# Kernel optimization log

Measured on AMD Instinct MI355X. Metric: run time of the kernel, lower is better.

The kernel has to match this reference:

```python
import jax, jax.numpy as jnp
import numpy as np

N, D, T, H, R = 1024, 6, 60, 64, 64
NEG = -10000.0
SLOPE = 0.01  # default LeakyReLU negative slope


def setup_inputs() -> dict:
    key = jax.random.key(0)
    ks = jax.random.split(key, 12)
    x = jax.random.normal(ks[0], (N, D * T), jnp.float32)
    relation_matrix = (jax.random.uniform(ks[1], (N, N, R)) < 0.02).astype(jnp.float32)
    s = 1.0 / np.sqrt(H)
    inp = {
        "x": x,
        "relation_matrix": relation_matrix,
        "W": jax.random.normal(ks[2], (2 * H + R, 1), jnp.float32) / np.sqrt(2 * H + R),
        "b": jnp.zeros((), jnp.float32),
        "fc_w": jax.random.normal(ks[3], (1, 2 * H), jnp.float32) * s,
        "fc_b": jnp.zeros((1,), jnp.float32),
        "Wih0": jax.random.normal(ks[4], (3 * H, D), jnp.float32) * s,
        "Whh0": jax.random.normal(ks[5], (3 * H, H), jnp.float32) * s,
        "bih0": jax.random.normal(ks[6], (3 * H,), jnp.float32) * s,
        "bhh0": jax.random.normal(ks[7], (3 * H,), jnp.float32) * s,
        "Wih1": jax.random.normal(ks[8], (3 * H, H), jnp.float32) * s,
        "Whh1": jax.random.normal(ks[9], (3 * H, H), jnp.float32) * s,
        "bih1": jax.random.normal(ks[10], (3 * H,), jnp.float32) * s,
        "bhh1": jax.random.normal(ks[11], (3 * H,), jnp.float32) * s,
    }
    return inp


def gru_layer(x, Wih, Whh, bih, bhh):
    # x: [N, T, in] -> outputs [N, T, H]; torch GRU gate order: r, z, n
    xg = x @ Wih.T + bih            # [N, T, 3H], input gates precomputed
    xg = jnp.swapaxes(xg, 0, 1)     # [T, N, 3H]

    def step(h, g):
        hg = h @ Whh.T + bhh
        xr, xz, xn = jnp.split(g, 3, axis=-1)
        hr, hz, hn = jnp.split(hg, 3, axis=-1)
        r = jax.nn.sigmoid(xr + hr)
        z = jax.nn.sigmoid(xz + hz)
        n = jnp.tanh(xn + r * hn)
        h = (1.0 - z) * n + z * h
        return h, h

    h0 = jnp.zeros((x.shape[0], Whh.shape[1]), x.dtype)
    _, ys = jax.lax.scan(step, h0, xg)
    return jnp.swapaxes(ys, 0, 1)   # [N, T, H]


def reference(x, relation_matrix, W, b, fc_w, fc_b,
              Wih0, Whh0, bih0, bhh0, Wih1, Whh1, bih1, bhh1):
    # [N, D*T] -> [N, T, D]
    xs = jnp.transpose(x.reshape(x.shape[0], D, -1), (0, 2, 1))
    h = gru_layer(xs, Wih0, Whh0, bih0, bhh0)
    h = gru_layer(h, Wih1, Whh1, bih1, bhh1)
    h = h[:, -1, :]                 # [N, H] last-step hidden

    # score[i,j] = cat(h_i, h_j, rel_ij) @ W + b, computed without the NxNx(2H+R) concat
    Wv = W[:, 0]
    sa = h @ Wv[:H]                              # [N]  (ei part)
    sb = h @ Wv[H:2 * H]                         # [N]  (hidden_batch part)
    sr = jnp.einsum('ijr,r->ij', relation_matrix, Wv[2 * H:])  # [N, N]
    weight = sa[:, None] + sb[None, :] + sr + b
    weight = jnp.where(weight >= 0, weight, SLOPE * weight)    # LeakyReLU

    mask = (relation_matrix.sum(-1) != 0).astype(h.dtype)      # [N, N]
    temp = mask * weight
    temp = jnp.where(temp == 0, NEG, temp)                     # faithful to torch ==0 fill
    valid = jax.nn.softmax(temp, axis=1) * mask

    agg = valid @ h                                            # [N, H]
    hidden = jnp.concatenate([h, agg], axis=1)                 # [N, 2H]
    pred_all = (hidden @ fc_w.T + fc_b).squeeze()
    return pred_all
```

## Files before the change

### kernel.cpp

```cpp
#include <hip/hip_runtime.h>
#include <cstddef>

#define NN 1024
#define DD 6
#define TT 60
#define HH 64
#define NEGV  (-10000.0f)
#define SLOPEV (0.01f)
#define GRUB 64
#define RELB 896

#define PRZ 0
#define PXN 2432
#define PHN 3648
#define HF0 4864
#define HF1 6080
#define BH0 7296
#define BH1 7872
#define XH  8448
#define SMEMF 12288

typedef _Float16 v8h __attribute__((ext_vector_type(8)));
typedef float    v4f __attribute__((ext_vector_type(4)));

#define MF(a, b, c) __builtin_amdgcn_mfma_f32_16x16x32_f16((a), (b), (c), 0, 0, 0)

__device__ __forceinline__ float sig_(float x)  { return 1.0f / (1.0f + __expf(-x)); }
__device__ __forceinline__ float tanh_(float x) { return 1.0f - 2.0f / (__expf(2.0f * x) + 1.0f); }
__device__ __forceinline__ float bcf_(const float a, const float b) {
    return __builtin_bit_cast(float, __builtin_amdgcn_cvt_pkrtz(a, b));
}
__device__ __forceinline__ v8h zero8() {
    v8h r;
    #pragma unroll
    for (int j = 0; j < 8; ++j) r[j] = (_Float16)0.f;
    return r;
}
__device__ __forceinline__ v8h pack8(const float* __restrict__ p) {
    v8h r;
    #pragma unroll
    for (int j = 0; j < 8; ++j) r[j] = (_Float16)p[j];
    return r;
}
__device__ __forceinline__ v8h pack6(const float* __restrict__ p) {
    v8h r = zero8();
    #pragma unroll
    for (int j = 0; j < 6; ++j) r[j] = (_Float16)p[j];
    return r;
}

__global__ __launch_bounds__(256, 1)
void k_main(const float* __restrict__ x, const float* __restrict__ rel,
            const float* __restrict__ W, const float* __restrict__ fc_w,
            const float* __restrict__ Wih0, const float* __restrict__ Whh0,
            const float* __restrict__ bih0, const float* __restrict__ bhh0,
            const float* __restrict__ Wih1, const float* __restrict__ Whh1,
            const float* __restrict__ bih1, const float* __restrict__ bhh1,
            float* __restrict__ sa, float* __restrict__ sb,
            float* __restrict__ hdot, float* __restrict__ hb,
            float* __restrict__ sr, float* __restrict__ ssum)
{
    __shared__ float smem[SMEMF];
    const int tid = threadIdx.x;

    if (blockIdx.x >= GRUB) {
        const float* __restrict__ Wv = W + 2 * HH;
        const unsigned base = (unsigned)(blockIdx.x - GRUB) * 256 + tid;
        for (unsigned p = base; p < (unsigned)(NN * NN); p += (unsigned)RELB * 256) {
            const float4* b4 = (const float4*)(rel + (size_t)p * 64);
            float4 v[16];
            #pragma unroll
            for (int q = 0; q < 16; ++q) v[q] = b4[q];
            float d0 = 0.f, d1 = 0.f, s0 = 0.f, s1 = 0.f;
            #pragma unroll
            for (int q = 0; q < 16; ++q) {
                d0 += v[q].x * Wv[4*q]   + v[q].z * Wv[4*q+2];
                d1 += v[q].y * Wv[4*q+1] + v[q].w * Wv[4*q+3];
                s0 += v[q].x + v[q].z;
                s1 += v[q].y + v[q].w;
            }
            sr[p]   = d0 + d1;
            ssum[p] = s0 + s1;
        }
        return;
    }

    const int w    = tid >> 6;
    const int lane = tid & 63;
    const int quad = lane >> 4;
    const int mc   = lane & 15;
    const int nb   = blockIdx.x * 16;

    for (int idx = tid; idx < TT * 16; idx += 256) {
        const int t = idx >> 4, n = idx & 15;
        const float* xp = x + (size_t)(nb + n) * (DD * TT) + t;
        float4 pk;
        pk.x = bcf_(xp[0],   xp[60]);
        pk.y = bcf_(xp[120], xp[180]);
        pk.z = bcf_(xp[240], xp[300]);
        pk.w = 0.f;
        *(float4*)(smem + XH + idx * 4) = pk;
    }
    for (int idx = tid; idx < 1152; idx += 256) smem[BH0 + idx] = 0.f;
    for (int idx = tid; idx < 2432; idx += 256) smem[HF0 + idx] = 0.f;

    const int r0row = 16 * w + mc;
    const int zrow  = 64 + 16 * w + mc;
    const int nrow  = 128 + 16 * w + mc;
    const v8h Ar0 = pack8(Whh0 + (size_t)r0row * HH + quad * 8);
    const v8h Ar1 = pack8(Whh0 + (size_t)r0row * HH + 32 + quad * 8);
    const v8h Az0 = pack8(Whh0 + (size_t)zrow  * HH + quad * 8);
    const v8h Az1 = pack8(Whh0 + (size_t)zrow  * HH + 32 + quad * 8);
    const v8h An0 = pack8(Whh0 + (size_t)nrow  * HH + quad * 8);
    const v8h An1 = pack8(Whh0 + (size_t)nrow  * HH + 32 + quad * 8);
    v8h Arx = zero8(), Azx = zero8(), Anx = zero8();
    if (quad == 0) {
        Arx = pack6(Wih0 + r0row * DD);
        Azx = pack6(Wih0 + zrow  * DD);
        Anx = pack6(Wih0 + nrow  * DD);
    }
    const v8h R0 = pack8(Wih1 + (size_t)r0row * HH + quad * 8);
    const v8h R1 = pack8(Wih1 + (size_t)r0row * HH + 32 + quad * 8);
    const v8h R2 = pack8(Whh1 + (size_t)r0row * HH + quad * 8);
    const v8h R3 = pack8(Whh1 + (size_t)r0row * HH + 32 + quad * 8);
    const v8h Z0 = pack8(Wih1 + (size_t)zrow * HH + quad * 8);
    const v8h Z1 = pack8(Wih1 + (size_t)zrow * HH + 32 + quad * 8);
    const v8h Z2 = pack8(Whh1 + (size_t)zrow * HH + quad * 8);
    const v8h Z3 = pack8(Whh1 + (size_t)zrow * HH + 32 + quad * 8);
    const v8h Nx0 = pack8(Wih1 + (size_t)nrow * HH + quad * 8);
    const v8h Nx1 = pack8(Wih1 + (size_t)nrow * HH + 32 + quad * 8);
    const v8h Nh0 = pack8(Whh1 + (size_t)nrow * HH + quad * 8);
    const v8h Nh1 = pack8(Whh1 + (size_t)nrow * HH + 32 + quad * 8);

    float bR0[4], bZ0v[4], bXn0[4], bHn0[4], bR1[4], bZ1v[4], bXn1[4], bHn1[4];
    #pragma unroll
    for (int e = 0; e < 4; ++e) {
        const int cr = 16 * w + quad * 4 + e;
        bR0[e]  = bih0[cr] + bhh0[cr];
        bZ0v[e] = bih0[64 + cr] + bhh0[64 + cr];
        bXn0[e] = bih0[128 + cr];
        bHn0[e] = bhh0[128 + cr];
        bR1[e]  = bih1[cr] + bhh1[cr];
        bZ1v[e] = bih1[64 + cr] + bhh1[64 + cr];
        bXn1[e] = bih1[128 + cr];
        bHn1[e] = bhh1[128 + cr];
    }
    __syncthreads();

    auto ldb = [&](int BH, int win) -> v8h {
        return __builtin_bit_cast(v8h,
            *(const float4*)(smem + BH + mc * 36 + win * 16 + quad * 4));
    };
    auto stC = [&](int base, int rowbase, v4f c) {
        #pragma unroll
        for (int e = 0; e < 4; ++e)
            smem[base + (rowbase + quad * 4 + e) * 19 + mc] = c[e];
    };
    auto upd = [&](int HF, int BH) {
        const int n = tid & 15, jb = (tid >> 4) * 4;
        float hv[4];
        #pragma unroll
        for (int e = 0; e < 4; ++e) {
            const int j = jb + e;
            const float rp = smem[PRZ + j * 19 + n];
            const float zp = smem[PRZ + (64 + j) * 19 + n];
            const float xn = smem[PXN + j * 19 + n];
            const float hn = smem[PHN + j * 19 + n];
            const float hp = smem[HF + j * 19 + n];
            const float r  = sig_(rp), z = sig_(zp);
            const float nv = tanh_(xn + r * hn);
            const float h  = (1.f - z) * nv + z * hp;
            smem[HF + j * 19 + n] = h;
            hv[e] = h;
        }
        float2 pk;
        pk.x = bcf_(hv[0], hv[1]);
        pk.y = bcf_(hv[2], hv[3]);
        *(float2*)(smem + BH + n * 36 + (jb >> 1)) = pk;
    };

    for (int t = 0; t < TT; ++t) {
        {
            const v8h b0 = ldb(BH0, 0);
            const v8h b1 = ldb(BH0, 1);
            const float4 xl = *(const float4*)(smem + XH + (t * 16 + mc) * 4);
            v8h bx = zero8();
            if (quad == 0) bx = __builtin_bit_cast(v8h, xl);

            v4f c = {bR0[0], bR0[1], bR0[2], bR0[3]};
            c = MF(Ar0, b0, c); c = MF(Ar1, b1, c); c = MF(Arx, bx, c);
            stC(PRZ, 16 * w, c);
            v4f cz = {bZ0v[0], bZ0v[1], bZ0v[2], bZ0v[3]};
            cz = MF(Az0, b0, cz); cz = MF(Az1, b1, cz); cz = MF(Azx, bx, cz);
            stC(PRZ, 64 + 16 * w, cz);
            v4f ch = {bHn0[0], bHn0[1], bHn0[2], bHn0[3]};
            ch = MF(An0, b0, ch); ch = MF(An1, b1, ch);
            stC(PHN, 16 * w, ch);
            v4f cx = {bXn0[0], bXn0[1], bXn0[2], bXn0[3]};
            cx = MF(Anx, bx, cx);
            stC(PXN, 16 * w, cx);
        }
        __syncthreads();
        upd(HF0, BH0);
        __syncthreads();
        {
            const v8h g0 = ldb(BH0, 0);
            const v8h g1 = ldb(BH0, 1);
            const v8h g2 = ldb(BH1, 0);
            const v8h g3 = ldb(BH1, 1);

            v4f c = {bR1[0], bR1[1], bR1[2], bR1[3]};
            c = MF(R0, g0, c); c = MF(R1, g1, c); c = MF(R2, g2, c); c = MF(R3, g3, c);
            stC(PRZ, 16 * w, c);
            v4f cz = {bZ1v[0], bZ1v[1], bZ1v[2], bZ1v[3]};
            cz = MF(Z0, g0, cz); cz = MF(Z1, g1, cz); cz = MF(Z2, g2, cz); cz = MF(Z3, g3, cz);
            stC(PRZ, 64 + 16 * w, cz);
            v4f cx = {bXn1[0], bXn1[1], bXn1[2], bXn1[3]};
            cx = MF(Nx0, g0, cx); cx = MF(Nx1, g1, cx);
            stC(PXN, 16 * w, cx);
            v4f ch = {bHn1[0], bHn1[1], bHn1[2], bHn1[3]};
            ch = MF(Nh0, g2, ch); ch = MF(Nh1, g3, ch);
            stC(PHN, 16 * w, ch);
        }
        __syncthreads();
        upd(HF1, BH1);
        __syncthreads();
    }

    {
        const int n = lane >> 2, p = lane & 3;
        const float* __restrict__ wp = (w == 0) ? W : (w == 1) ? (W + HH)
                                     : (w == 2) ? fc_w : (fc_w + HH);
        float v = 0.f;
        #pragma unroll
        for (int q = 0; q < 16; ++q) {
            const int j = p * 16 + q;
            v += smem[HF1 + j * 19 + n] * wp[j];
        }
        v += __shfl_down(v, 2);
        v += __shfl_down(v, 1);
        if (p == 0) {
            float* dst = (w == 0) ? sa : (w == 1) ? sb : (w == 2) ? hdot : hb;
            dst[nb + n] = v;
        }
    }
}

__global__ __launch_bounds__(256)
void k2(const float* __restrict__ sa, const float* __restrict__ sb,
        const float* __restrict__ hdot, const float* __restrict__ hb,
        const float* __restrict__ sr, const float* __restrict__ ssum,
        const float* __restrict__ bscal, const float* __restrict__ fc_b,
        float* __restrict__ out)
{
    __shared__ float red[12];
    const int i   = blockIdx.x;
    const int tid = threadIdx.x;
    const int j4  = tid * 4;
    const float sai = sa[i] + bscal[0];

    const float4 srv = *(const float4*)(sr   + (size_t)i * NN + j4);
    const float4 ssv = *(const float4*)(ssum + (size_t)i * NN + j4);
    const float4 sbv = *(const float4*)(sb + j4);

    float tv[4], mk[4];
    float mloc = -3.4e38f;
    {
        const float srq[4] = {srv.x, srv.y, srv.z, srv.w};
        const float ssq[4] = {ssv.x, ssv.y, ssv.z, ssv.w};
        const float sbq[4] = {sbv.x, sbv.y, sbv.z, sbv.w};
        #pragma unroll
        for (int q = 0; q < 4; ++q) {
            float wv = sai + sbq[q] + srq[q];
            wv = (wv >= 0.0f) ? wv : SLOPEV * wv;
            const float m = (ssq[q] != 0.0f) ? 1.0f : 0.0f;
            float tt = m * wv;
            tt = (tt == 0.0f) ? NEGV : tt;
            tv[q] = tt; mk[q] = m;
            mloc = fmaxf(mloc, tt);
        }
    }
    #pragma unroll
    for (int off = 32; off >= 1; off >>= 1) mloc = fmaxf(mloc, __shfl_xor(mloc, off));
    if ((tid & 63) == 0) red[tid >> 6] = mloc;
    __syncthreads();
    const float mx = fmaxf(fmaxf(red[0], red[1]), fmaxf(red[2], red[3]));

    const float4 hbv = *(const float4*)(hb + j4);
    const float hbq[4] = {hbv.x, hbv.y, hbv.z, hbv.w};
    float sloc = 0.0f, vloc = 0.0f;
    #pragma unroll
    for (int q = 0; q < 4; ++q) {
        const float e = __expf(tv[q] - mx);
        sloc += e;
        vloc += e * mk[q] * hbq[q];
    }
    #pragma unroll
    for (int off = 32; off >= 1; off >>= 1) {
        sloc += __shfl_xor(sloc, off);
        vloc += __shfl_xor(vloc, off);
    }
    if ((tid & 63) == 0) { red[4 + (tid >> 6)] = sloc; red[8 + (tid >> 6)] = vloc; }
    __syncthreads();
    if (tid == 0) {
        const float denom = red[4] + red[5] + red[6] + red[7];
        const float vsum  = red[8] + red[9] + red[10] + red[11];
        out[i] = hdot[i] + vsum / denom + fc_b[0];
    }
}

extern "C" void kernel_launch(void* const* d_in, const int* in_sizes, int n_in,
                              void* d_out, int out_size, void* d_ws, size_t ws_size,
                              hipStream_t stream)
{
    const float* x     = (const float*)d_in[0];
    const float* rel   = (const float*)d_in[1];
    const float* W     = (const float*)d_in[2];
    const float* b     = (const float*)d_in[3];
    const float* fc_w  = (const float*)d_in[4];
    const float* fc_b  = (const float*)d_in[5];
    const float* Wih0  = (const float*)d_in[6];
    const float* Whh0  = (const float*)d_in[7];
    const float* bih0  = (const float*)d_in[8];
    const float* bhh0  = (const float*)d_in[9];
    const float* Wih1  = (const float*)d_in[10];
    const float* Whh1  = (const float*)d_in[11];
    const float* bih1  = (const float*)d_in[12];
    const float* bhh1  = (const float*)d_in[13];

    float* ws   = (float*)d_ws;
    float* sa   = ws;
    float* sb   = sa   + NN;
    float* hdot = sb   + NN;
    float* hb   = hdot + NN;
    float* sr   = hb   + NN;
    float* ssum = sr   + (size_t)NN * NN;

    k_main<<<GRUB + RELB, 256, 0, stream>>>(x, rel, W, fc_w,
                                            Wih0, Whh0, bih0, bhh0,
                                            Wih1, Whh1, bih1, bhh1,
                                            sa, sb, hdot, hb, sr, ssum);
    k2<<<NN, 256, 0, stream>>>(sa, sb, hdot, hb, sr, ssum,
                               b, fc_b, (float*)d_out);
}
```

Measured before the change: 436.0 us.

## Pipeline GRU layers across wavefront groups with 512-thread blocks

Doubles the block to 512 threads. Warps 0-3 run GRU layer 0 at step i while warps 4-7 run layer 1 at step i-1, each with its own preactivation buffers in shared memory. This halves the number of barrier phases per timestep, removing the serial dependence between the two layers within a step. The relation-reduction blocks also grow to 512 threads, which raises register pressure with no minimum-occupancy hint and increases shared memory per block.

```diff
diff --git a/kernel.cpp b/kernel.cpp
--- a/kernel.cpp
+++ b/kernel.cpp
@@ -10,15 +10,18 @@
 #define GRUB 64
 #define RELB 896
 
-#define PRZ 0
-#define PXN 2432
-#define PHN 3648
-#define HF0 4864
-#define HF1 6080
-#define BH0 7296
-#define BH1 7872
-#define XH  8448
-#define SMEMF 12288
+#define PA_RZ 0
+#define PA_XN 2432
+#define PA_HN 3648
+#define PB_RZ 4864
+#define PB_XN 7296
+#define PB_HN 8512
+#define HF0   9728
+#define HF1   10944
+#define BH0   12160
+#define BH1   12736
+#define XH    13312
+#define SMEMF 17152
 
 typedef _Float16 v8h __attribute__((ext_vector_type(8)));
 typedef float    v4f __attribute__((ext_vector_type(4)));
@@ -49,7 +52,7 @@
     return r;
 }
 
-__global__ __launch_bounds__(256, 1)
+__global__ __launch_bounds__(512)
 void k_main(const float* __restrict__ x, const float* __restrict__ rel,
             const float* __restrict__ W, const float* __restrict__ fc_w,
             const float* __restrict__ Wih0, const float* __restrict__ Whh0,
@@ -65,8 +68,8 @@
 
     if (blockIdx.x >= GRUB) {
         const float* __restrict__ Wv = W + 2 * HH;
-        const unsigned base = (unsigned)(blockIdx.x - GRUB) * 256 + tid;
-        for (unsigned p = base; p < (unsigned)(NN * NN); p += (unsigned)RELB * 256) {
+        const unsigned base = (unsigned)(blockIdx.x - GRUB) * 512 + tid;
+        for (unsigned p = base; p < (unsigned)(NN * NN); p += (unsigned)RELB * 512) {
             const float4* b4 = (const float4*)(rel + (size_t)p * 64);
             float4 v[16];
             #pragma unroll
@@ -90,8 +93,10 @@
     const int quad = lane >> 4;
     const int mc   = lane & 15;
     const int nb   = blockIdx.x * 16;
-
-    for (int idx = tid; idx < TT * 16; idx += 256) {
+    const bool isL0 = (w < 4);
+    const int wt   = isL0 ? w : (w - 4);
+
+    for (int idx = tid; idx < TT * 16; idx += 512) {
         const int t = idx >> 4, n = idx & 15;
         const float* xp = x + (size_t)(nb + n) * (DD * TT) + t;
         float4 pk;
@@ -101,49 +106,58 @@
         pk.w = 0.f;
         *(float4*)(smem + XH + idx * 4) = pk;
     }
-    for (int idx = tid; idx < 1152; idx += 256) smem[BH0 + idx] = 0.f;
-    for (int idx = tid; idx < 2432; idx += 256) smem[HF0 + idx] = 0.f;
-
-    const int r0row = 16 * w + mc;
-    const int zrow  = 64 + 16 * w + mc;
-    const int nrow  = 128 + 16 * w + mc;
-    const v8h Ar0 = pack8(Whh0 + (size_t)r0row * HH + quad * 8);
-    const v8h Ar1 = pack8(Whh0 + (size_t)r0row * HH + 32 + quad * 8);
-    const v8h Az0 = pack8(Whh0 + (size_t)zrow  * HH + quad * 8);
-    const v8h Az1 = pack8(Whh0 + (size_t)zrow  * HH + 32 + quad * 8);
-    const v8h An0 = pack8(Whh0 + (size_t)nrow  * HH + quad * 8);
-    const v8h An1 = pack8(Whh0 + (size_t)nrow  * HH + 32 + quad * 8);
-    v8h Arx = zero8(), Azx = zero8(), Anx = zero8();
-    if (quad == 0) {
-        Arx = pack6(Wih0 + r0row * DD);
-        Azx = pack6(Wih0 + zrow  * DD);
-        Anx = pack6(Wih0 + nrow  * DD);
-    }
-    const v8h R0 = pack8(Wih1 + (size_t)r0row * HH + quad * 8);
-    const v8h R1 = pack8(Wih1 + (size_t)r0row * HH + 32 + quad * 8);
-    const v8h R2 = pack8(Whh1 + (size_t)r0row * HH + quad * 8);
-    const v8h R3 = pack8(Whh1 + (size_t)r0row * HH + 32 + quad * 8);
-    const v8h Z0 = pack8(Wih1 + (size_t)zrow * HH + quad * 8);
-    const v8h Z1 = pack8(Wih1 + (size_t)zrow * HH + 32 + quad * 8);
-    const v8h Z2 = pack8(Whh1 + (size_t)zrow * HH + quad * 8);
-    const v8h Z3 = pack8(Whh1 + (size_t)zrow * HH + 32 + quad * 8);
-    const v8h Nx0 = pack8(Wih1 + (size_t)nrow * HH + quad * 8);
-    const v8h Nx1 = pack8(Wih1 + (size_t)nrow * HH + 32 + quad * 8);
-    const v8h Nh0 = pack8(Whh1 + (size_t)nrow * HH + quad * 8);
-    const v8h Nh1 = pack8(Whh1 + (size_t)nrow * HH + 32 + quad * 8);
-
-    float bR0[4], bZ0v[4], bXn0[4], bHn0[4], bR1[4], bZ1v[4], bXn1[4], bHn1[4];
+    for (int idx = tid; idx < 1152; idx += 512) smem[BH0 + idx] = 0.f;
+    for (int idx = tid; idx < 2432; idx += 512) smem[HF0 + idx] = 0.f;
+
+    const int r0row = 16 * wt + mc;
+    const int zrow  = 64 + 16 * wt + mc;
+    const int nrow  = 128 + 16 * wt + mc;
+    v8h F0 = zero8(), F1 = zero8(), F2 = zero8(), F3 = zero8();
+    v8h F4 = zero8(), F5 = zero8(), F6 = zero8(), F7 = zero8();
+    v8h F8 = zero8(), F9 = zero8(), F10 = zero8(), F11 = zero8();
+    v8h Xr = zero8(), Xz = zero8(), Xn = zero8();
+    if (isL0) {
+        F0 = pack8(Whh0 + (size_t)r0row * HH + quad * 8);
+        F1 = pack8(Whh0 + (size_t)r0row * HH + 32 + quad * 8);
+        F2 = pack8(Whh0 + (size_t)zrow  * HH + quad * 8);
+        F3 = pack8(Whh0 + (size_t)zrow  * HH + 32 + quad * 8);
+        F4 = pack8(Whh0 + (size_t)nrow  * HH + quad * 8);
+        F5 = pack8(Whh0 + (size_t)nrow  * HH + 32 + quad * 8);
+        if (quad == 0) {
+            Xr = pack6(Wih0 + r0row * DD);
+            Xz = pack6(Wih0 + zrow  * DD);
+            Xn = pack6(Wih0 + nrow  * DD);
+        }
+    } else {
+        F0 = pack8(Wih1 + (size_t)r0row * HH + quad * 8);
+        F1 = pack8(Wih1 + (size_t)r0row * HH + 32 + quad * 8);
+        F2 = pack8(Whh1 + (size_t)r0row * HH + quad * 8);
+        F3 = pack8(Whh1 + (size_t)r0row * HH + 32 + quad * 8);
+        F4 = pack8(Wih1 + (size_t)zrow * HH + quad * 8);
+        F5 = pack8(Wih1 + (size_t)zrow * HH + 32 + quad * 8);
+        F6 = pack8(Whh1 + (size_t)zrow * HH + quad * 8);
+        F7 = pack8(Whh1 + (size_t)zrow * HH + 32 + quad * 8);
+        F8 = pack8(Wih1 + (size_t)nrow * HH + quad * 8);
+        F9 = pack8(Wih1 + (size_t)nrow * HH + 32 + quad * 8);
+        F10 = pack8(Whh1 + (size_t)nrow * HH + quad * 8);
+        F11 = pack8(Whh1 + (size_t)nrow * HH + 32 + quad * 8);
+    }
+
+    float bR[4], bZ[4], bXn[4], bHn[4];
     #pragma unroll
     for (int e = 0; e < 4; ++e) {
-        const int cr = 16 * w + quad * 4 + e;
-        bR0[e]  = bih0[cr] + bhh0[cr];
-        bZ0v[e] = bih0[64 + cr] + bhh0[64 + cr];
-        bXn0[e] = bih0[128 + cr];
-        bHn0[e] = bhh0[128 + cr];
-        bR1[e]  = bih1[cr] + bhh1[cr];
-        bZ1v[e] = bih1[64 + cr] + bhh1[64 + cr];
-        bXn1[e] = bih1[128 + cr];
-        bHn1[e] = bhh1[128 + cr];
+        const int cr = 16 * wt + quad * 4 + e;
+        if (isL0) {
+            bR[e]  = bih0[cr] + bhh0[cr];
+            bZ[e]  = bih0[64 + cr] + bhh0[64 + cr];
+            bXn[e] = bih0[128 + cr];
+            bHn[e] = bhh0[128 + cr];
+        } else {
+            bR[e]  = bih1[cr] + bhh1[cr];
+            bZ[e]  = bih1[64 + cr] + bhh1[64 + cr];
+            bXn[e] = bih1[128 + cr];
+            bHn[e] = bhh1[128 + cr];
+        }
     }
     __syncthreads();
 
@@ -156,8 +170,8 @@
         for (int e = 0; e < 4; ++e)
             smem[base + (rowbase + quad * 4 + e) * 19 + mc] = c[e];
     };
-    auto upd = [&](int HF, int BH) {
-        const int n = tid & 15, jb = (tid >> 4) * 4;
+    auto upd = [&](int PRZ, int PXN, int PHN, int HF, int BH, int lt) {
+        const int n = lt & 15, jb = (lt >> 4) * 4;
         float hv[4];
         #pragma unroll
         for (int e = 0; e < 4; ++e) {
@@ -179,55 +193,59 @@
         *(float2*)(smem + BH + n * 36 + (jb >> 1)) = pk;
     };
 
-    for (int t = 0; t < TT; ++t) {
-        {
-            const v8h b0 = ldb(BH0, 0);
-            const v8h b1 = ldb(BH0, 1);
-            const float4 xl = *(const float4*)(smem + XH + (t * 16 + mc) * 4);
-            v8h bx = zero8();
-            if (quad == 0) bx = __builtin_bit_cast(v8h, xl);
-
-            v4f c = {bR0[0], bR0[1], bR0[2], bR0[3]};
-            c = MF(Ar0, b0, c); c = MF(Ar1, b1, c); c = MF(Arx, bx, c);
-            stC(PRZ, 16 * w, c);
-            v4f cz = {bZ0v[0], bZ0v[1], bZ0v[2], bZ0v[3]};
-            cz = MF(Az0, b0, cz); cz = MF(Az1, b1, cz); cz = MF(Azx, bx, cz);
-            stC(PRZ, 64 + 16 * w, cz);
-            v4f ch = {bHn0[0], bHn0[1], bHn0[2], bHn0[3]};
-            ch = MF(An0, b0, ch); ch = MF(An1, b1, ch);
-            stC(PHN, 16 * w, ch);
-            v4f cx = {bXn0[0], bXn0[1], bXn0[2], bXn0[3]};
-            cx = MF(Anx, bx, cx);
-            stC(PXN, 16 * w, cx);
+    for (int i = 0; i <= TT; ++i) {
+        if (isL0) {
+            if (i < TT) {
+                const v8h b0 = ldb(BH0, 0);
+                const v8h b1 = ldb(BH0, 1);
+                const float4 xl = *(const float4*)(smem + XH + (i * 16 + mc) * 4);
+                v8h bx = zero8();
+                if (quad == 0) bx = __builtin_bit_cast(v8h, xl);
+
+                v4f c = {bR[0], bR[1], bR[2], bR[3]};
+                c = MF(F0, b0, c); c = MF(F1, b1, c); c = MF(Xr, bx, c);
+                stC(PA_RZ, 16 * wt, c);
+                v4f cz = {bZ[0], bZ[1], bZ[2], bZ[3]};
+                cz = MF(F2, b0, cz); cz = MF(F3, b1, cz); cz = MF(Xz, bx, cz);
+                stC(PA_RZ, 64 + 16 * wt, cz);
+                v4f ch = {bHn[0], bHn[1], bHn[2], bHn[3]};
+                ch = MF(F4, b0, ch); ch = MF(F5, b1, ch);
+                stC(PA_HN, 16 * wt, ch);
+                v4f cx = {bXn[0], bXn[1], bXn[2], bXn[3]};
+                cx = MF(Xn, bx, cx);
+                stC(PA_XN, 16 * wt, cx);
+            }
+        } else {
+            if (i >= 1) {
+                const v8h g0 = ldb(BH0, 0);
+                const v8h g1 = ldb(BH0, 1);
+                const v8h g2 = ldb(BH1, 0);
+                const v8h g3 = ldb(BH1, 1);
+
+                v4f c = {bR[0], bR[1], bR[2], bR[3]};
+                c = MF(F0, g0, c); c = MF(F1, g1, c); c = MF(F2, g2, c); c = MF(F3, g3, c);
+                stC(PB_RZ, 16 * wt, c);
+                v4f cz = {bZ[0], bZ[1], bZ[2], bZ[3]};
+                cz = MF(F4, g0, cz); cz = MF(F5, g1, cz); cz = MF(F6, g2, cz); cz = MF(F7, g3, cz);
+                stC(PB_RZ, 64 + 16 * wt, cz);
+                v4f cx = {bXn[0], bXn[1], bXn[2], bXn[3]};
+                cx = MF(F8, g0, cx); cx = MF(F9, g1, cx);
+                stC(PB_XN, 16 * wt, cx);
+                v4f ch = {bHn[0], bHn[1], bHn[2], bHn[3]};
+                ch = MF(F10, g2, ch); ch = MF(F11, g3, ch);
+                stC(PB_HN, 16 * wt, ch);
+            }
         }
         __syncthreads();
-        upd(HF0, BH0);
+        if (tid < 256) {
+            if (i < TT) upd(PA_RZ, PA_XN, PA_HN, HF0, BH0, tid);
+        } else {
+            if (i >= 1) upd(PB_RZ, PB_XN, PB_HN, HF1, BH1, tid - 256);
+        }
         __syncthreads();
-        {
-            const v8h g0 = ldb(BH0, 0);
-            const v8h g1 = ldb(BH0, 1);
-            const v8h g2 = ldb(BH1, 0);
-            const v8h g3 = ldb(BH1, 1);
-
-            v4f c = {bR1[0], bR1[1], bR1[2], bR1[3]};
-            c = MF(R0, g0, c); c = MF(R1, g1, c); c = MF(R2, g2, c); c = MF(R3, g3, c);
-            stC(PRZ, 16 * w, c);
-            v4f cz = {bZ1v[0], bZ1v[1], bZ1v[2], bZ1v[3]};
-            cz = MF(Z0, g0, cz); cz = MF(Z1, g1, cz); cz = MF(Z2, g2, cz); cz = MF(Z3, g3, cz);
-            stC(PRZ, 64 + 16 * w, cz);
-            v4f cx = {bXn1[0], bXn1[1], bXn1[2], bXn1[3]};
-            cx = MF(Nx0, g0, cx); cx = MF(Nx1, g1, cx);
-            stC(PXN, 16 * w, cx);
-            v4f ch = {bHn1[0], bHn1[1], bHn1[2], bHn1[3]};
-            ch = MF(Nh0, g2, ch); ch = MF(Nh1, g3, ch);
-            stC(PHN, 16 * w, ch);
-        }
-        __syncthreads();
-        upd(HF1, BH1);
-        __syncthreads();
-    }
-
-    {
+    }
+
+    if (w < 4) {
         const int n = lane >> 2, p = lane & 3;
         const float* __restrict__ wp = (w == 0) ? W : (w == 1) ? (W + HH)
                                      : (w == 2) ? fc_w : (fc_w + HH);
@@ -336,7 +354,7 @@
     float* sr   = hb   + NN;
     float* ssum = sr   + (size_t)NN * NN;
 
-    k_main<<<GRUB + RELB, 256, 0, stream>>>(x, rel, W, fc_w,
+    k_main<<<GRUB + RELB, 512, 0, stream>>>(x, rel, W, fc_w,
                                             Wih0, Whh0, bih0, bhh0,
                                             Wih1, Whh1, bih1, bhh1,
                                             sa, sb, hdot, hb, sr, ssum);
```

Result: faster. 386.7 us (-11.3%).
